# Optimization experiments

Hardware: AMD Instinct MI355X
Metric: run time of the kernel (lower is better)

## Reference

```python
import jax, jax.numpy as jnp
import numpy as np

jax.config.update("jax_enable_x64", True)

# Dims (see shape_source): batch, heads, q-len, kv-len, head-channels, quant group
B, H, T, S, HC = 2, 16, 1024, 1024, 128
G = 8            # group_size from A/R_QUANT_PARAMS
SCALE_SHIFT = 14 # combined dequant shift applied to integer QK scores before softmax
O_SM = 14        # fixed-point offset of the integer softmax output (LUT-style)
PROB_QMAX = 255.0  # 8-bit unsigned probability mantissa (R_QUANT_PARAMS n_bits=8)


def _dequant_po2(q, s):
    """q: int mantissas [..., N], s: nonneg po2 shift exponents [..., N//G].
    Emulates (q << s) per group of G channels (pot_scale activation quantizer)."""
    s_full = jnp.repeat(s, G, axis=-1)
    return q.astype(jnp.float64) * jnp.exp2(s_full.astype(jnp.float64))


def setup_inputs() -> dict:
    key = jax.random.key(0)
    ks = jax.random.split(key, 6)
    # signed 8-bit mantissas in [-128, 127]
    q_q = jax.random.randint(ks[0], (B, H, T, HC), 0, 256, dtype=jnp.int32) - 128
    k_q = jax.random.randint(ks[1], (B, H, S, HC), 0, 256, dtype=jnp.int32) - 128
    vt_q = jax.random.randint(ks[2], (B, H, HC, S), 0, 256, dtype=jnp.int32) - 128
    # nonnegative power-of-two shifts, one per group of G=8
    q_s = jax.random.randint(ks[3], (B, H, T, HC // G), 0, 4, dtype=jnp.int32)
    k_s = jax.random.randint(ks[4], (B, H, S, HC // G), 0, 4, dtype=jnp.int32)
    vt_s = jax.random.randint(ks[5], (B, H, HC, S // G), 0, 4, dtype=jnp.int32)
    return {"q_q": q_q, "q_s": q_s, "k_q": k_q, "k_s": k_s, "vt_q": vt_q, "vt_s": vt_s}


def reference(q_q, q_s, k_q, k_s, vt_q, vt_s):
    # ---- shift_qk_matmul: (q_q << q_s) @ (k_q << k_s)^T in float64, truncated to int64
    q = _dequant_po2(q_q, q_s)                       # [B,H,T,HC] f64
    k = _dequant_po2(k_q, k_s)                       # [B,H,S,HC] f64
    scores = jnp.einsum("bhtc,bhsc->bhts", q, k).astype(jnp.int64)

    # ---- integer softmax emulation: rescale integer scores, softmax, then
    # re-quantize probabilities with an 8-bit per-group (G=8 along S) po2 scale
    logits = scores.astype(jnp.float32) * np.float32(2.0 ** (-SCALE_SHIFT) / np.sqrt(HC))
    p = jax.nn.softmax(logits, axis=-1)              # [B,H,T,S]
    val = jnp.round(p * (2.0 ** O_SM))               # fixed-point probs (ints)
    vg = val.reshape(B, H, T, S // G, G)
    gmax = jnp.max(vg, axis=-1, keepdims=True)
    r_shift = jnp.clip(jnp.ceil(jnp.log2(jnp.maximum(gmax, 1.0) / PROB_QMAX)), 0.0, None)
    r_q = jnp.clip(jnp.round(vg / jnp.exp2(r_shift)), 0.0, PROB_QMAX)
    r = (r_q * jnp.exp2(r_shift)).reshape(B, H, T, S).astype(jnp.float64)  # (r_q << r_s)

    # ---- shift_rv_matmul: r @ (vt_q << vt_s)^T in float64, truncated to int64
    vt = _dequant_po2(vt_q, vt_s)                    # [B,H,HC,S] f64
    a = jnp.einsum("bhts,bhcs->bhtc", r, vt).astype(jnp.int64)  # [B,H,T,HC]
    return a
```

## Files before the change

kernel.cpp:

```cpp
#include <hip/hip_runtime.h>
#include <string.h>


typedef int   v4i __attribute__((ext_vector_type(4)));
typedef float v4f __attribute__((ext_vector_type(4)));
typedef short v8s __attribute__((ext_vector_type(8)));
typedef unsigned v2u __attribute__((ext_vector_type(2)));

#define BHN 32
#define TN  1024
#define SN  1024
#define HCN 128
#define TT  16
#define KD_BH 262144
#define VD_BH 262144
#define WS_NEED ((size_t)BHN*(KD_BH+VD_BH))

__device__ __forceinline__ unsigned short bf16_of_int(int v){
    return (unsigned short)(__float_as_uint((float)v) >> 16);
}

__device__ __forceinline__ v4i pack8(const int* __restrict__ p, int s){
    unsigned wd[4];
    #pragma unroll
    for (int j=0;j<4;j++){
        int a = p[j*2]   << s;
        int b = p[j*2+1] << s;
        wd[j] = (unsigned)bf16_of_int(a) | ((unsigned)bf16_of_int(b) << 16);
    }
    return v4i{(int)wd[0],(int)wd[1],(int)wd[2],(int)wd[3]};
}

__global__ __launch_bounds__(256) void digitize(
    const int* __restrict__ k_q, const int* __restrict__ k_s,
    const int* __restrict__ vt_q, const int* __restrict__ vt_s,
    unsigned char* __restrict__ kd, unsigned char* __restrict__ vd)
{
    const int w    = threadIdx.x >> 6;
    const int lane = threadIdx.x & 63;
    const int l15  = lane & 15;
    const int q4   = lane >> 4;
    const int task = blockIdx.x*4 + w;
    if (task < 8192){
        const int kc = task & 3, n = (task>>2)&7, ch = (task>>5)&7, bh = task>>8;
        const int row = bh*SN + ch*128 + n*16 + l15;
        const int col = kc*32 + q4*8;
        v4i f = pack8(k_q + (size_t)row*HCN + col, k_s[row*16 + (col>>3)]);
        size_t base = (size_t)bh*KD_BH + (size_t)((((ch*8+n)*4 + kc)*64 + lane)*16);
        *(v4i*)(kd + base) = f;
    } else {
        const int t  = task - 8192;
        const int n  = t & 7, kb = (t>>3)&31, bh = t>>8;
        const int row = bh*HCN + n*16 + l15;
        v4i f = pack8(vt_q + (size_t)row*SN + kb*32 + q4*8,
                      vt_s[row*128 + kb*4 + q4]);
        size_t base = (size_t)bh*VD_BH + (size_t)(((kb*8 + n)*64 + lane)*16);
        *(v4i*)(vd + base) = f;
    }
}

template<bool PK>
__global__ __launch_bounds__(256,4) void mha_mfma(
    const int* __restrict__ q_q, const int* __restrict__ q_s,
    const int* __restrict__ k_q, const int* __restrict__ k_s,
    const int* __restrict__ vt_q, const int* __restrict__ vt_s,
    const unsigned char* __restrict__ kd, const unsigned char* __restrict__ vd,
    int* __restrict__ out)
{
    __shared__ __align__(16) unsigned short rbuf[16*1024];
    float* redm = (float*)(rbuf + 16128);
    float* redf = (float*)(rbuf + 16256);

    const int tid  = threadIdx.x;
    const int ln   = tid & 15;
    const int qd4  = (tid >> 4) & 3;
    const int w    = tid >> 6;
    const int lane = tid & 63;
    const int blk = blockIdx.x;
    const int bh  = ((blk>>9)<<3) | (blk&7);
    const int t0  = ((blk>>3)&63) * TT;

    v8s qf[4];
    {
        const int* qrow = q_q + (size_t)(bh*TN + t0 + ln)*HCN;
        const int* qs   = q_s + (size_t)(bh*TN + t0 + ln)*16;
        #pragma unroll
        for (int kc=0; kc<4; ++kc){
            int col = kc*32 + qd4*8;
            v4i t = pack8(qrow + col, qs[col>>3]);
            memcpy(&qf[kc], &t, 16);
        }
    }

    v4f scv[16];

    const v4i* kb_ = (const v4i*)(kd + (size_t)bh*KD_BH);
    for (int ch=0; ch<8; ++ch){
        #pragma unroll
        for (int i=0;i<2;i++){
            const int n = w*2 + i;
            v4f acc{0.f,0.f,0.f,0.f};
            #pragma unroll
            for (int kc=0;kc<4;kc++){
                v8s af;
                if (PK){
                    v4i a_ = kb_[((ch*8+n)*4 + kc)*64 + lane];
                    memcpy(&af, &a_, 16);
                } else {
                    int srow = bh*SN + ch*128 + n*16 + ln;
                    int cc   = kc*32 + qd4*8;
                    v4i a_ = pack8(k_q + (size_t)srow*HCN + cc,
                                   k_s[srow*16 + (cc>>3)]);
                    memcpy(&af, &a_, 16);
                }
                acc = __builtin_amdgcn_mfma_f32_16x16x32_bf16(af, qf[kc], acc, 0,0,0);
            }
            scv[ch*2 + i] = acc;
        }
    }

    const float CS2 = (float)(6.103515625e-05 / 11.313708498984760390566
                              * 1.4426950408889634074);
    {
        float m0=-3.0e38f, m1=-3.0e38f, m2=-3.0e38f, m3=-3.0e38f;
        #pragma unroll
        for (int st=0;st<16;st++){
            m0 = fmaxf(m0, scv[st][0]);
            m1 = fmaxf(m1, scv[st][1]);
            m2 = fmaxf(m2, scv[st][2]);
            m3 = fmaxf(m3, scv[st][3]);
        }
        float m_ = fmaxf(fmaxf(m0,m1), fmaxf(m2,m3));
        m_ = fmaxf(m_, __shfl_xor(m_, 16));
        m_ = fmaxf(m_, __shfl_xor(m_, 32));
        if ((tid & 48) == 0) redm[w*16 + ln] = m_;
    }
    __syncthreads();
    float inv14;
    {
        const float mrow = fmaxf(fmaxf(redm[ln], redm[16+ln]),
                                 fmaxf(redm[32+ln], redm[48+ln]));
        float s0=0.f, s1=0.f, s2=0.f, s3=0.f;
        #pragma unroll
        for (int st=0;st<16;st++){
            #pragma unroll
            for (int r=0;r<4;r++){
                float t_ = (scv[st][r] - mrow) * CS2;
                float e;
                asm("v_exp_f32 %0, %1" : "=v"(e) : "v"(t_));
                scv[st][r] = e;
                if (r==0) s0 += e; else if (r==1) s1 += e; else if (r==2) s2 += e; else s3 += e;
            }
        }
        float s_ = (s0+s1) + (s2+s3);
        s_ += __shfl_xor(s_, 16);
        s_ += __shfl_xor(s_, 32);
        if ((tid & 48) == 0) redf[w*16 + ln] = s_;
    }
    __syncthreads();
    {
        float sum = redf[ln] + redf[16+ln] + redf[32+ln] + redf[48+ln];
        inv14 = 16384.0f / sum;
    }
    __syncthreads();

    {
        const int lnr4 = (ln & 7) << 4;
        const int cbase = w*32 + qd4*4;
        unsigned short* rp = rbuf + ln*1024;
        #pragma unroll
        for (int st=0;st<16;st++){
            float v0 = rintf(scv[st][0] * inv14);
            float v1 = rintf(scv[st][1] * inv14);
            float v2 = rintf(scv[st][2] * inv14);
            float v3 = rintf(scv[st][3] * inv14);
            float g = fmaxf(fmaxf(v0,v1), fmaxf(v2,v3));
            g = fmaxf(g, __shfl_xor(g, 16));
            int gi = max((int)g, 1);
            int x  = gi - 1;
            int e2 = 31 - __clz(x | 255);
            int sh = (e2 - 7) + ((x >> (e2 - 7)) == 255);
            float isc = __int_as_float((127 - sh) << 23);
            float fsc = __int_as_float((127 + sh) << 23);
            unsigned b0 = __float_as_uint(rintf(v0*isc) * fsc);
            unsigned b1 = __float_as_uint(rintf(v1*isc) * fsc);
            unsigned b2 = __float_as_uint(rintf(v2*isc) * fsc);
            unsigned b3 = __float_as_uint(rintf(v3*isc) * fsc);
            unsigned w0 = __builtin_amdgcn_perm(b1, b0, 0x07060302u);
            unsigned w1 = __builtin_amdgcn_perm(b3, b2, 0x07060302u);
            int c0 = (st>>1)*128 + cbase + (st&1)*16;
            *(v2u*)(rp + (c0 ^ lnr4)) = v2u{w0, w1};
        }
    }
    __syncthreads();

    const v4i* vb = (const v4i*)(vd + (size_t)bh*VD_BH);
    const unsigned short* rp2 = rbuf + ln*1024;
    const int lnr4b = (ln & 7) << 4;
    v4f acc0{0,0,0,0}, acc1{0,0,0,0};
    #pragma unroll 4
    for (int kb=0; kb<32; ++kb){
        v8s af = *(const v8s*)(rp2 + ((kb*32 + qd4*8) ^ lnr4b));
        v4i b0, b1;
        if (PK){
            b0 = vb[(kb*8 + w*2    )*64 + lane];
            b1 = vb[(kb*8 + w*2 + 1)*64 + lane];
        } else {
            #pragma unroll
            for (int i=0;i<2;i++){
                int chan = (w*2+i)*16 + ln;
                v4i t = pack8(vt_q + (size_t)(bh*HCN + chan)*SN + kb*32 + qd4*8,
                              vt_s[(bh*HCN + chan)*128 + kb*4 + qd4]);
                if (i==0) b0 = t; else b1 = t;
            }
        }
        v8s bs0, bs1;
        memcpy(&bs0, &b0, 16);
        memcpy(&bs1, &b1, 16);
        acc0 = __builtin_amdgcn_mfma_f32_16x16x32_bf16(af, bs0, acc0, 0,0,0);
        acc1 = __builtin_amdgcn_mfma_f32_16x16x32_bf16(af, bs1, acc1, 0,0,0);
    }
    #pragma unroll
    for (int r=0;r<4;r++){
        size_t o = (size_t)(bh*TN + t0 + qd4*4 + r)*HCN + w*32 + ln;
        out[o]      = (int)rintf(acc0[r]);
        out[o + 16] = (int)rintf(acc1[r]);
    }
}

extern "C" void kernel_launch(void* const* d_in, const int* in_sizes, int n_in,
                              void* d_out, int out_size, void* d_ws, size_t ws_size,
                              hipStream_t stream) {
    const int* q_q  = (const int*)d_in[0];
    const int* q_s  = (const int*)d_in[1];
    const int* k_q  = (const int*)d_in[2];
    const int* k_s  = (const int*)d_in[3];
    const int* vt_q = (const int*)d_in[4];
    const int* vt_s = (const int*)d_in[5];
    int* out = (int*)d_out;

    unsigned char* kd = (unsigned char*)d_ws;
    unsigned char* vd = kd + (size_t)BHN*KD_BH;

    if (ws_size >= WS_NEED){
        digitize<<<dim3(4096), 256, 0, stream>>>(k_q,k_s,vt_q,vt_s, kd,vd);
        mha_mfma<true><<<dim3(2048), 256, 0, stream>>>(
            q_q,q_s,k_q,k_s,vt_q,vt_s, kd,vd, out);
    } else {
        mha_mfma<false><<<dim3(2048), 256, 0, stream>>>(
            q_q,q_s,k_q,k_s,vt_q,vt_s, kd,vd, out);
    }
}
```

Before: 154.7 us.

## Double-buffer K and V fragment loads into registers with sched barriers

Adds explicit register double-buffering for the packed K fragments in the QK phase and the V and probability fragments in the RV phase, prefetching the next tile while MFMAs run on the current one. The first V tiles are prefetched before the probability quantization step so their global load latency overlaps that work. sched_barrier calls keep the compiler from reordering loads past the MFMAs, and launch bounds drop from 4 to 3 waves per SIMD to leave room for the extra registers. The cost is lower occupancy and higher register pressure.

```diff
diff --git a/kernel.cpp b/kernel.cpp
--- a/kernel.cpp
+++ b/kernel.cpp
@@ -60,7 +60,7 @@
 }
 
 template<bool PK>
-__global__ __launch_bounds__(256,4) void mha_mfma(
+__global__ __launch_bounds__(256,3) void mha_mfma(
     const int* __restrict__ q_q, const int* __restrict__ q_s,
     const int* __restrict__ k_q, const int* __restrict__ k_s,
     const int* __restrict__ vt_q, const int* __restrict__ vt_s,
@@ -95,27 +95,49 @@
     v4f scv[16];
 
     const v4i* kb_ = (const v4i*)(kd + (size_t)bh*KD_BH);
-    for (int ch=0; ch<8; ++ch){
-        #pragma unroll
-        for (int i=0;i<2;i++){
-            const int n = w*2 + i;
+    if (PK){
+        v4i fb[2][4];
+        {
+            const v4i* ta = kb_ + ((w*2)*4)*64 + lane;
+            fb[0][0]=ta[0]; fb[0][1]=ta[64]; fb[0][2]=ta[128]; fb[0][3]=ta[192];
+        }
+        #pragma unroll
+        for (int t=0; t<16; ++t){
+            const int par = t & 1;
+            if (t < 15){
+                const int t1 = t+1, ch1 = t1>>1, i1 = t1&1;
+                const v4i* ta = kb_ + ((ch1*8 + w*2 + i1)*4)*64 + lane;
+                fb[par^1][0]=ta[0];   fb[par^1][1]=ta[64];
+                fb[par^1][2]=ta[128]; fb[par^1][3]=ta[192];
+            }
+            __builtin_amdgcn_sched_barrier(0);
             v4f acc{0.f,0.f,0.f,0.f};
             #pragma unroll
             for (int kc=0;kc<4;kc++){
                 v8s af;
-                if (PK){
-                    v4i a_ = kb_[((ch*8+n)*4 + kc)*64 + lane];
-                    memcpy(&af, &a_, 16);
-                } else {
+                memcpy(&af, &fb[par][kc], 16);
+                acc = __builtin_amdgcn_mfma_f32_16x16x32_bf16(af, qf[kc], acc, 0,0,0);
+            }
+            scv[t] = acc;
+        }
+    } else {
+        for (int ch=0; ch<8; ++ch){
+            #pragma unroll
+            for (int i=0;i<2;i++){
+                const int n = w*2 + i;
+                v4f acc{0.f,0.f,0.f,0.f};
+                #pragma unroll
+                for (int kc=0;kc<4;kc++){
                     int srow = bh*SN + ch*128 + n*16 + ln;
                     int cc   = kc*32 + qd4*8;
                     v4i a_ = pack8(k_q + (size_t)srow*HCN + cc,
                                    k_s[srow*16 + (cc>>3)]);
+                    v8s af;
                     memcpy(&af, &a_, 16);
+                    acc = __builtin_amdgcn_mfma_f32_16x16x32_bf16(af, qf[kc], acc, 0,0,0);
                 }
-                acc = __builtin_amdgcn_mfma_f32_16x16x32_bf16(af, qf[kc], acc, 0,0,0);
-            }
-            scv[ch*2 + i] = acc;
+                scv[ch*2 + i] = acc;
+            }
         }
     }
 
@@ -163,6 +185,18 @@
         inv14 = 16384.0f / sum;
     }
     __syncthreads();
+
+    const v4i* vb = (const v4i*)(vd + (size_t)bh*VD_BH);
+    v4i gb[2][8];
+    v8s ga[2][4];
+    if (PK){
+        #pragma unroll
+        for (int j=0;j<4;j++){
+            gb[0][j*2]   = vb[(j*8 + w*2    )*64 + lane];
+            gb[0][j*2+1] = vb[(j*8 + w*2 + 1)*64 + lane];
+        }
+        __builtin_amdgcn_sched_barrier(0);
+    }
 
     {
         const int lnr4 = (ln & 7) << 4;
@@ -194,18 +228,40 @@
     }
     __syncthreads();
 
-    const v4i* vb = (const v4i*)(vd + (size_t)bh*VD_BH);
     const unsigned short* rp2 = rbuf + ln*1024;
     const int lnr4b = (ln & 7) << 4;
     v4f acc0{0,0,0,0}, acc1{0,0,0,0};
-    #pragma unroll 4
-    for (int kb=0; kb<32; ++kb){
-        v8s af = *(const v8s*)(rp2 + ((kb*32 + qd4*8) ^ lnr4b));
-        v4i b0, b1;
-        if (PK){
-            b0 = vb[(kb*8 + w*2    )*64 + lane];
-            b1 = vb[(kb*8 + w*2 + 1)*64 + lane];
-        } else {
+    if (PK){
+        #pragma unroll
+        for (int j=0;j<4;j++)
+            ga[0][j] = *(const v8s*)(rp2 + ((j*32 + qd4*8) ^ lnr4b));
+        #pragma unroll
+        for (int g=0; g<8; ++g){
+            const int par = g & 1;
+            if (g < 7){
+                #pragma unroll
+                for (int j=0;j<4;j++){
+                    int kb = (g+1)*4 + j;
+                    gb[par^1][j*2]   = vb[(kb*8 + w*2    )*64 + lane];
+                    gb[par^1][j*2+1] = vb[(kb*8 + w*2 + 1)*64 + lane];
+                    ga[par^1][j] = *(const v8s*)(rp2 + ((kb*32 + qd4*8) ^ lnr4b));
+                }
+            }
+            __builtin_amdgcn_sched_barrier(0);
+            #pragma unroll
+            for (int j=0;j<4;j++){
+                v8s bs0, bs1;
+                memcpy(&bs0, &gb[par][j*2],   16);
+                memcpy(&bs1, &gb[par][j*2+1], 16);
+                acc0 = __builtin_amdgcn_mfma_f32_16x16x32_bf16(ga[par][j], bs0, acc0, 0,0,0);
+                acc1 = __builtin_amdgcn_mfma_f32_16x16x32_bf16(ga[par][j], bs1, acc1, 0,0,0);
+            }
+        }
+    } else {
+        #pragma unroll 4
+        for (int kb=0; kb<32; ++kb){
+            v8s af = *(const v8s*)(rp2 + ((kb*32 + qd4*8) ^ lnr4b));
+            v4i b0, b1;
             #pragma unroll
             for (int i=0;i<2;i++){
                 int chan = (w*2+i)*16 + ln;
@@ -213,12 +269,12 @@
                               vt_s[(bh*HCN + chan)*128 + kb*4 + qd4]);
                 if (i==0) b0 = t; else b1 = t;
             }
-        }
-        v8s bs0, bs1;
-        memcpy(&bs0, &b0, 16);
-        memcpy(&bs1, &b1, 16);
-        acc0 = __builtin_amdgcn_mfma_f32_16x16x32_bf16(af, bs0, acc0, 0,0,0);
-        acc1 = __builtin_amdgcn_mfma_f32_16x16x32_bf16(af, bs1, acc1, 0,0,0);
+            v8s bs0, bs1;
+            memcpy(&bs0, &b0, 16);
+            memcpy(&bs1, &b1, 16);
+            acc0 = __builtin_amdgcn_mfma_f32_16x16x32_bf16(af, bs0, acc0, 0,0,0);
+            acc1 = __builtin_amdgcn_mfma_f32_16x16x32_bf16(af, bs1, acc1, 0,0,0);
+        }
     }
     #pragma unroll
     for (int r=0;r<4;r++){
```

After: 146.8 us. 5.1% less time.
